# Optimization experiments

Measured on AMD Instinct MI355X. Metric: run time of the kernel, lower is better.

## Reference

```python
import jax, jax.numpy as jnp
import numpy as np

T, NP, NA, NV = 8, 16000, 16000, 200
DIN, H, KA, L = 256, 256, 4, 5
YEARS_TRAIN = (5, 6, 7)
BETA, EPS = 0.5, 1.0
SQRT2 = 1.4142135623730951


def setup_inputs() -> dict:
    key = jax.random.key(0)
    ks = jax.random.split(key, 24)
    s = 0.05
    return {
        'x_paper': jax.random.normal(ks[0], (T, NP, DIN), jnp.float32),
        'x_author': jax.random.normal(ks[1], (T, NA, DIN), jnp.float32),
        'x_venue': jax.random.normal(ks[2], (T, NV, DIN), jnp.float32),
        'neigh_author_idx': jax.random.randint(ks[3], (NP, KA), 0, NA),
        'neigh_venue_idx': jax.random.randint(ks[4], (NP,), 0, NV),
        'y_true': jax.random.uniform(ks[5], (len(YEARS_TRAIN), NP, L), jnp.float32, 0.0, 50.0),
        'W_paper': s * jax.random.normal(ks[6], (DIN, H), jnp.float32),
        'b_paper': jnp.zeros((H,), jnp.float32),
        'W_author': s * jax.random.normal(ks[7], (DIN, H), jnp.float32),
        'b_author': jnp.zeros((H,), jnp.float32),
        'W_venue': s * jax.random.normal(ks[8], (DIN, H), jnp.float32),
        'b_venue': jnp.zeros((H,), jnp.float32),
        'w_meta': jax.random.normal(ks[9], (3,), jnp.float32),
        'Wx': s * jax.random.normal(ks[10], (H, 3 * H), jnp.float32),
        'Wh': s * jax.random.normal(ks[11], (H, 3 * H), jnp.float32),
        'b_gru': jnp.zeros((3 * H,), jnp.float32),
        'W_eta': s * jax.random.normal(ks[12], (H, 1), jnp.float32),
        'b_eta': jnp.zeros((1,), jnp.float32),
        'W_mu': s * jax.random.normal(ks[13], (H, 1), jnp.float32),
        'b_mu': jnp.zeros((1,), jnp.float32),
        'W_sigma': s * jax.random.normal(ks[14], (H, 1), jnp.float32),
        'b_sigma': jnp.zeros((1,), jnp.float32),
    }


def reference(x_paper, x_author, x_venue, neigh_author_idx, neigh_venue_idx, y_true,
              W_paper, b_paper, W_author, b_author, W_venue, b_venue, w_meta,
              Wx, Wh, b_gru, W_eta, b_eta, W_mu, b_mu, W_sigma, b_sigma):
    # --- encoder: per-type linear + ReLU over all T snapshots ---
    emb_p = jax.nn.relu(jnp.einsum('tnd,dh->tnh', x_paper, W_paper) + b_paper)   # [T,NP,H]
    emb_a = jax.nn.relu(jnp.einsum('tnd,dh->tnh', x_author, W_author) + b_author)  # [T,NA,H]
    emb_v = jax.nn.relu(jnp.einsum('tnd,dh->tnh', x_venue, W_venue) + b_venue)   # [T,NV,H]

    # --- temporal smoothing regulariser L_time (all nodes common across years) ---
    l_time = jnp.mean(jnp.stack([
        jnp.mean(jnp.sum((e[1:] - e[:-1]) ** 2, axis=-1)) for e in (emb_p, emb_a, emb_v)
    ]))

    # --- weighted imputer, batched over all papers and all years ---
    w = jax.nn.softmax(w_meta)
    auth_mean = jnp.mean(emb_a[:, neigh_author_idx], axis=2)   # [T,NP,H]
    ven = emb_v[:, neigh_venue_idx]                            # [T,NP,H]
    v_all = w[0] * auth_mean + w[1] * ven + w[2] * emb_p       # [T,NP,H]

    # --- build lookback sequences V_p for all train years at once ---
    yrs = np.array([[t - k for k in range(1, L + 1)] for t in YEARS_TRAIN])  # [3,L]
    V = jnp.transpose(v_all[yrs], (0, 2, 1, 3)).reshape(-1, L, H)  # [B=3*NP, L, H]
    B = V.shape[0]

    # --- ImpactRNN: GRU over the lookback sequence ---
    def gru_step(h, x):
        gx = x @ Wx + b_gru
        gh = h @ Wh
        xr, xz, xn = jnp.split(gx, 3, axis=-1)
        hr, hz, hn = jnp.split(gh, 3, axis=-1)
        r = jax.nn.sigmoid(xr + hr)
        z = jax.nn.sigmoid(xz + hz)
        n = jnp.tanh(xn + r * hn)
        return (1.0 - z) * n + z * h, None

    h0 = jnp.zeros((B, H), V.dtype)
    h_last, _ = jax.lax.scan(gru_step, h0, jnp.swapaxes(V, 0, 1))

    eta = jax.nn.softplus(h_last @ W_eta + b_eta)              # [B,1]
    mu = h_last @ W_mu + b_mu                                  # [B,1]
    sigma = jax.nn.softplus(h_last @ W_sigma + b_sigma) + 1e-3  # [B,1]

    # --- cumulative log-normal citation curve, then per-horizon increments ---
    horizons = jnp.arange(1.0, L + 1.0, dtype=V.dtype)
    zscore = (jnp.log(horizons)[None, :] - mu) / (sigma * SQRT2)
    y_cum = eta * 0.5 * (1.0 + jax.lax.erf(zscore))            # [B,L]
    y_hat = jnp.concatenate([y_cum[:, :1], y_cum[:, 1:] - y_cum[:, :-1]], axis=1)

    l_pred = jnp.mean((jnp.log1p(y_true.reshape(-1, L) + EPS) - jnp.log1p(y_hat)) ** 2)
    return l_pred + BETA * l_time
```

## Files before the change

kernel.cpp:

```cpp
#include <hip/hip_runtime.h>
#include <cmath>

#define NP  16000
#define NV  200
#define HH  256

typedef short short8 __attribute__((ext_vector_type(8)));
typedef float f32x4  __attribute__((ext_vector_type(4)));

__device__ __forceinline__ unsigned short f2b(float f) {
  union { float f; unsigned u; } x; x.f = f;
  unsigned r = x.u + 0x7fffu + ((x.u >> 16) & 1u);
  return (unsigned short)(r >> 16);
}
__device__ __forceinline__ float b2f(unsigned short h) {
  union { unsigned u; float f; } x; x.u = ((unsigned)h) << 16;
  return x.f;
}
__device__ __forceinline__ float b2f_lo(unsigned u) {
  union { unsigned v; float f; } x; x.v = u << 16; return x.f;
}
__device__ __forceinline__ float b2f_hi(unsigned u) {
  union { unsigned v; float f; } x; x.v = u & 0xffff0000u; return x.f;
}
__device__ __forceinline__ unsigned cvt2(float a, float b) {
  unsigned r;
  asm("v_cvt_pk_bf16_f32 %0, %1, %2" : "=v"(r) : "v"(a), "v"(b));
  return r;
}
__device__ __forceinline__ void gld16(const void* g, void* l) {
  __builtin_amdgcn_global_load_lds((const __attribute__((address_space(1))) void*)g,
                                   (__attribute__((address_space(3))) void*)l, 16, 0, 0);
}
__device__ __forceinline__ float sigm(float x) { return 1.f / (1.f + __expf(-x)); }
__device__ __forceinline__ float tanhfast(float x) {
  const float e = __expf(-2.f * fabsf(x));
  const float t = (1.f - e) / (1.f + e);
  return x < 0.f ? -t : t;
}
__device__ __forceinline__ int xcd_swz(int orig, int q, int r) {
  const int xcd = orig & 7, loc = orig >> 3;
  return (xcd < r ? xcd * (q + 1) : r * (q + 1) + (xcd - r) * q) + loc;
}

__global__ __launch_bounds__(256) void packWt(const float* __restrict__ W,
                                              unsigned short* __restrict__ Wt) {
  const int n = blockIdx.x, k = threadIdx.x;
  Wt[n * 256 + k] = f2b(W[k * 256 + n]);
}
__global__ __launch_bounds__(256) void packW2t(const float* __restrict__ Wx,
                                               const float* __restrict__ Wh,
                                               unsigned short* __restrict__ W2t) {
  const int col = blockIdx.x;
  for (int k = threadIdx.x; k < 512; k += 256)
    W2t[(size_t)col * 512 + k] =
        f2b(k < 256 ? Wx[(size_t)k * 768 + col] : Wh[(size_t)(k - 256) * 768 + col]);
}

__global__ __launch_bounds__(512) void embed_all(
    const float* __restrict__ Xp, const float* __restrict__ Xa, const float* __restrict__ Xv,
    const unsigned short* __restrict__ Wtp, const unsigned short* __restrict__ Wta,
    const unsigned short* __restrict__ Wtv,
    const float* __restrict__ bp, const float* __restrict__ ba, const float* __restrict__ bvn,
    unsigned short* __restrict__ Ep, unsigned short* __restrict__ Ea,
    unsigned short* __restrict__ Ev) {
  __shared__ __align__(16) unsigned short lds[20480];
  unsigned short* As = lds;
  unsigned short* Bs = lds + 4096;
  const int t = threadIdx.x, w = t >> 6, l = t & 63;
  const int bid = blockIdx.x;
  const float* Xf; const unsigned short* Wt; const float* bias; unsigned short* E;
  int m0;
  if (bid < 2000)      { Xf = Xp; Wt = Wtp; bias = bp;  E = Ep; m0 = bid * 64; }
  else if (bid < 4000) { Xf = Xa; Wt = Wta; bias = ba;  E = Ea; m0 = (bid - 2000) * 64; }
  else                 { Xf = Xv; Wt = Wtv; bias = bvn; E = Ev; m0 = (bid - 4000) * 64; }
  const int srow = l >> 3, scol = ((l & 7) ^ srow) * 8;
  const int wrow = (w >> 2) * 32, wcol = (w & 3) * 64;
  const int arow = t >> 3, aseg = t & 7;
  const float* aptr = Xf + (size_t)(m0 + arow) * 256 + aseg * 8;

  f32x4 acc[2][4];
#pragma unroll
  for (int i = 0; i < 2; ++i)
#pragma unroll
    for (int j = 0; j < 4; ++j) acc[i][j] = {0.f, 0.f, 0.f, 0.f};

  float4 a0 = *reinterpret_cast<const float4*>(aptr);
  float4 a1 = *reinterpret_cast<const float4*>(aptr + 4);

#pragma unroll
  for (int c = 0; c < 4; ++c) {
#pragma unroll
    for (int i = 0; i < 4; ++i) {
      const int seg = 4 * w + i;
      gld16(Wt + (size_t)(8 * seg + srow) * 256 + c * 64 + scol, (void*)(Bs + seg * 512));
    }
    {
      uint4 u;
      u.x = cvt2(a0.x, a0.y); u.y = cvt2(a0.z, a0.w);
      u.z = cvt2(a1.x, a1.y); u.w = cvt2(a1.z, a1.w);
      const int slot = aseg ^ (arow & 7);
      *reinterpret_cast<uint4*>(As + arow * 64 + slot * 8) = u;
    }
    if (c < 3) {
      const float* np = aptr + (c + 1) * 64;
      a0 = *reinterpret_cast<const float4*>(np);
      a1 = *reinterpret_cast<const float4*>(np + 4);
    }
    __syncthreads();
#pragma unroll
    for (int ks = 0; ks < 2; ++ks) {
      short8 av[2], bv[4];
#pragma unroll
      for (int mi = 0; mi < 2; ++mi) {
        const int r = wrow + mi * 16 + (l & 15);
        const int slot = (ks * 4 + (l >> 4)) ^ (r & 7);
        av[mi] = *reinterpret_cast<const short8*>(As + r * 64 + slot * 8);
      }
#pragma unroll
      for (int nj = 0; nj < 4; ++nj) {
        const int r = wcol + nj * 16 + (l & 15);
        const int slot = (ks * 4 + (l >> 4)) ^ (r & 7);
        bv[nj] = *reinterpret_cast<const short8*>(Bs + r * 64 + slot * 8);
      }
#pragma unroll
      for (int mi = 0; mi < 2; ++mi)
#pragma unroll
        for (int nj = 0; nj < 4; ++nj)
          acc[mi][nj] = __builtin_amdgcn_mfma_f32_16x16x32_bf16(av[mi], bv[nj], acc[mi][nj], 0, 0, 0);
    }
    __syncthreads();
  }

#pragma unroll
  for (int nj = 0; nj < 4; ++nj) {
    const int col = wcol + nj * 16 + (l & 15);
    const float bvv = bias[col];
#pragma unroll
    for (int mi = 0; mi < 2; ++mi)
#pragma unroll
      for (int e = 0; e < 4; ++e) {
        const int row = wrow + mi * 16 + (l >> 4) * 4 + e;
        lds[row * 264 + col] = f2b(fmaxf(acc[mi][nj][e] + bvv, 0.f));
      }
  }
  __syncthreads();
  {
    const int r2 = t >> 3, s2 = t & 7;
    const unsigned short* src = lds + r2 * 264 + s2 * 32;
    const uint4 v0 = *reinterpret_cast<const uint4*>(src);
    const uint4 v1 = *reinterpret_cast<const uint4*>(src + 8);
    const uint4 v2 = *reinterpret_cast<const uint4*>(src + 16);
    const uint4 v3 = *reinterpret_cast<const uint4*>(src + 24);
    uint4* dst = reinterpret_cast<uint4*>(E + (size_t)(m0 + r2) * 256 + s2 * 32);
    dst[0] = v0; dst[1] = v1; dst[2] = v2; dst[3] = v3;
  }
}

__global__ __launch_bounds__(512) void gx_gemm(const unsigned short* __restrict__ Abf,
                                               const unsigned short* __restrict__ W2t,
                                               const float* __restrict__ bias,
                                               unsigned short* __restrict__ GX) {
  __shared__ __align__(16) unsigned short lds[20480];
  unsigned short* As = lds;
  unsigned short* Bs = lds + 4096;
  const int t = threadIdx.x, w = t >> 6, l = t & 63;
  const int work = xcd_swz(blockIdx.x, 656, 2);
  const int m0 = (work / 3) * 64, n0 = (work % 3) * 256;
  const int srow = l >> 3, scol = ((l & 7) ^ srow) * 8;
  const int wrow = (w >> 2) * 32, wcol = (w & 3) * 64;

  f32x4 acc[2][4];
#pragma unroll
  for (int i = 0; i < 2; ++i)
#pragma unroll
    for (int j = 0; j < 4; ++j) acc[i][j] = {0.f, 0.f, 0.f, 0.f};

#pragma unroll
  for (int c = 0; c < 4; ++c) {
    gld16(Abf + (size_t)(m0 + 8 * w + srow) * 256 + c * 64 + scol, (void*)(As + w * 512));
#pragma unroll
    for (int i = 0; i < 4; ++i) {
      const int seg = 4 * w + i;
      gld16(W2t + (size_t)(n0 + 8 * seg + srow) * 512 + c * 64 + scol, (void*)(Bs + seg * 512));
    }
    __syncthreads();
#pragma unroll
    for (int ks = 0; ks < 2; ++ks) {
      short8 av[2], bv[4];
#pragma unroll
      for (int mi = 0; mi < 2; ++mi) {
        const int r = wrow + mi * 16 + (l & 15);
        const int slot = (ks * 4 + (l >> 4)) ^ (r & 7);
        av[mi] = *reinterpret_cast<const short8*>(As + r * 64 + slot * 8);
      }
#pragma unroll
      for (int nj = 0; nj < 4; ++nj) {
        const int r = wcol + nj * 16 + (l & 15);
        const int slot = (ks * 4 + (l >> 4)) ^ (r & 7);
        bv[nj] = *reinterpret_cast<const short8*>(Bs + r * 64 + slot * 8);
      }
#pragma unroll
      for (int mi = 0; mi < 2; ++mi)
#pragma unroll
        for (int nj = 0; nj < 4; ++nj)
          acc[mi][nj] = __builtin_amdgcn_mfma_f32_16x16x32_bf16(av[mi], bv[nj], acc[mi][nj], 0, 0, 0);
    }
    __syncthreads();
  }

#pragma unroll
  for (int nj = 0; nj < 4; ++nj) {
    const int col = wcol + nj * 16 + (l & 15);
    const float bvv = bias[n0 + col];
#pragma unroll
    for (int mi = 0; mi < 2; ++mi)
#pragma unroll
      for (int e = 0; e < 4; ++e) {
        const int row = wrow + mi * 16 + (l >> 4) * 4 + e;
        lds[row * 264 + col] = f2b(acc[mi][nj][e] + bvv);
      }
  }
  __syncthreads();
  {
    const int r2 = t >> 3, s2 = t & 7;
    const unsigned short* src = lds + r2 * 264 + s2 * 32;
    const uint4 v0 = *reinterpret_cast<const uint4*>(src);
    const uint4 v1 = *reinterpret_cast<const uint4*>(src + 8);
    const uint4 v2 = *reinterpret_cast<const uint4*>(src + 16);
    const uint4 v3 = *reinterpret_cast<const uint4*>(src + 24);
    uint4* dst = reinterpret_cast<uint4*>(GX + (size_t)(m0 + r2) * 768 + n0 + s2 * 32);
    dst[0] = v0; dst[1] = v1; dst[2] = v2; dst[3] = v3;
  }
}

__global__ __launch_bounds__(256) void ltime_kernel(const unsigned short* __restrict__ ep,
                                                    const unsigned short* __restrict__ ea,
                                                    const unsigned short* __restrict__ ev,
                                                    float* __restrict__ partials) {
  const unsigned PO = 3584000u, VO = 44800u;
  const unsigned TOT = 2u * PO + VO;
  const unsigned SL = 512000u, SLV = 6400u;
  const float wbig = 1.f / (3.f * 7.f * 16000.f);
  const float wsmall = 1.f / (3.f * 7.f * 200.f);
  float local = 0.f;
  for (unsigned i = blockIdx.x * 256u + threadIdx.x; i < TOT; i += gridDim.x * 256u) {
    const unsigned short* base; unsigned off, sl; float wgt;
    if (i < 2u * PO) { base = (i < PO) ? ep : ea; off = (i < PO) ? i : i - PO; sl = SL; wgt = wbig; }
    else             { base = ev; off = i - 2u * PO; sl = SLV; wgt = wsmall; }
    const uint4 u0 = *reinterpret_cast<const uint4*>(base + (size_t)off * 8);
    const uint4 u1 = *reinterpret_cast<const uint4*>(base + (size_t)(off + sl) * 8);
    float s = 0.f, d;
    d = b2f_lo(u1.x) - b2f_lo(u0.x); s += d * d;
    d = b2f_hi(u1.x) - b2f_hi(u0.x); s += d * d;
    d = b2f_lo(u1.y) - b2f_lo(u0.y); s += d * d;
    d = b2f_hi(u1.y) - b2f_hi(u0.y); s += d * d;
    d = b2f_lo(u1.z) - b2f_lo(u0.z); s += d * d;
    d = b2f_hi(u1.z) - b2f_hi(u0.z); s += d * d;
    d = b2f_lo(u1.w) - b2f_lo(u0.w); s += d * d;
    d = b2f_hi(u1.w) - b2f_hi(u0.w); s += d * d;
    local += wgt * s;
  }
  __shared__ float red[256];
  red[threadIdx.x] = local;
  __syncthreads();
  for (int s = 128; s > 0; s >>= 1) {
    if (threadIdx.x < s) red[threadIdx.x] += red[threadIdx.x + s];
    __syncthreads();
  }
  if (threadIdx.x == 0) partials[blockIdx.x] = red[0];
}

__global__ __launch_bounds__(256) void vall_kernel(const unsigned short* __restrict__ ep,
                                                   const unsigned short* __restrict__ ea,
                                                   const unsigned short* __restrict__ ev,
                                                   const int* __restrict__ aidx,
                                                   const int* __restrict__ vidx,
                                                   const float* __restrict__ wm,
                                                   unsigned short* __restrict__ vall) {
  const int w = threadIdx.x >> 6, l = threadIdx.x & 63;
  const int n = blockIdx.x * 4 + w;
  float w0 = wm[0], w1 = wm[1], w2 = wm[2];
  const float mx = fmaxf(w0, fmaxf(w1, w2));
  const float e0 = expf(w0 - mx), e1 = expf(w1 - mx), e2 = expf(w2 - mx);
  const float inv = 1.f / (e0 + e1 + e2);
  w0 = e0 * inv; w1 = e1 * inv; w2 = e2 * inv;
  const int a0 = aidx[n * 4 + 0], a1 = aidx[n * 4 + 1];
  const int a2 = aidx[n * 4 + 2], a3 = aidx[n * 4 + 3];
  const int vn = vidx[n];
  const int cb = l * 4;
  for (int t = 0; t < 7; ++t) {
    const size_t tb = (size_t)t * NP * HH;
    const uint2 ua0 = *reinterpret_cast<const uint2*>(ea + tb + (size_t)a0 * HH + cb);
    const uint2 ua1 = *reinterpret_cast<const uint2*>(ea + tb + (size_t)a1 * HH + cb);
    const uint2 ua2 = *reinterpret_cast<const uint2*>(ea + tb + (size_t)a2 * HH + cb);
    const uint2 ua3 = *reinterpret_cast<const uint2*>(ea + tb + (size_t)a3 * HH + cb);
    const uint2 uv  = *reinterpret_cast<const uint2*>(ev + (size_t)t * NV * HH + (size_t)vn * HH + cb);
    const uint2 up  = *reinterpret_cast<const uint2*>(ep + tb + (size_t)n * HH + cb);
    float o[4];
    o[0] = w0 * 0.25f * (b2f_lo(ua0.x) + b2f_lo(ua1.x) + b2f_lo(ua2.x) + b2f_lo(ua3.x)) + w1 * b2f_lo(uv.x) + w2 * b2f_lo(up.x);
    o[1] = w0 * 0.25f * (b2f_hi(ua0.x) + b2f_hi(ua1.x) + b2f_hi(ua2.x) + b2f_hi(ua3.x)) + w1 * b2f_hi(uv.x) + w2 * b2f_hi(up.x);
    o[2] = w0 * 0.25f * (b2f_lo(ua0.y) + b2f_lo(ua1.y) + b2f_lo(ua2.y) + b2f_lo(ua3.y)) + w1 * b2f_lo(uv.y) + w2 * b2f_lo(up.y);
    o[3] = w0 * 0.25f * (b2f_hi(ua0.y) + b2f_hi(ua1.y) + b2f_hi(ua2.y) + b2f_hi(ua3.y)) + w1 * b2f_hi(uv.y) + w2 * b2f_hi(up.y);
    uint2 ov; ov.x = cvt2(o[0], o[1]); ov.y = cvt2(o[2], o[3]);
    *reinterpret_cast<uint2*>(vall + tb + (size_t)n * HH + cb) = ov;
  }
}

__global__ __launch_bounds__(256) void gru_h0(const unsigned short* __restrict__ GX,
                                              unsigned short* __restrict__ H0) {
  const int idx = blockIdx.x * 256 + threadIdx.x;
  const int hrow = idx >> 6, jq = idx & 63;
  const int g = (hrow >= 32000) ? 2 : (hrow >= 16000 ? 1 : 0);
  const int n = hrow - g * 16000;
  const size_t gxrow = (size_t)(4 + g) * 16000 + n;
  const unsigned short* gp = GX + gxrow * 768 + jq * 4;
  const uint2 uz = *reinterpret_cast<const uint2*>(gp + 256);
  const uint2 un = *reinterpret_cast<const uint2*>(gp + 512);
  float h[4];
  h[0] = (1.f - sigm(b2f_lo(uz.x))) * tanhfast(b2f_lo(un.x));
  h[1] = (1.f - sigm(b2f_hi(uz.x))) * tanhfast(b2f_hi(un.x));
  h[2] = (1.f - sigm(b2f_lo(uz.y))) * tanhfast(b2f_lo(un.y));
  h[3] = (1.f - sigm(b2f_hi(uz.y))) * tanhfast(b2f_hi(un.y));
  uint2 o; o.x = cvt2(h[0], h[1]); o.y = cvt2(h[2], h[3]);
  *reinterpret_cast<uint2*>(H0 + (size_t)hrow * 256 + jq * 4) = o;
}

__global__ __launch_bounds__(512, 2) void gru_hstep(const unsigned short* __restrict__ GX,
                                                    const unsigned short* __restrict__ W2t,
                                                    const unsigned short* __restrict__ Hsrc,
                                                    unsigned short* __restrict__ Hdst,
                                                    int lstep) {
  __shared__ __align__(16) unsigned short lds[32768];
  unsigned short* As = lds;
  unsigned short* Bs = lds + 8192;
  const int t = threadIdx.x, w = t >> 6, l = t & 63;
  const int work = xcd_swz(blockIdx.x, 93, 6);
  const int bx = work >> 1, jb = work & 1;
  const int m0 = bx * 128, j0 = jb * 128;
  const int g = bx / 125;
  const size_t gxRowBase = (size_t)(4 + g - lstep) * 16000 + (size_t)(m0 - g * 16000);
  const int srow = l >> 3;
  const int scol = ((l & 7) ^ srow) * 8;
  const int wr = w >> 2, wj = w & 3;
  f32x4 acc[3][4][2];
#pragma unroll
  for (int gate = 0; gate < 3; ++gate)
#pragma unroll
    for (int mi = 0; mi < 4; ++mi)
#pragma unroll
      for (int nj = 0; nj < 2; ++nj) acc[gate][mi][nj] = {0.f, 0.f, 0.f, 0.f};

#pragma unroll
  for (int c = 0; c < 4; ++c) {
#pragma unroll
    for (int i = 0; i < 2; ++i) {
      const int seg = w * 2 + i;
      gld16(Hsrc + (size_t)(m0 + 8 * seg + srow) * 256 + c * 64 + scol, (void*)(As + seg * 512));
    }
#pragma unroll
    for (int i = 0; i < 6; ++i) {
      const int seg = w * 6 + i;
      const int tilerow = 8 * seg + srow;
      const int gate = tilerow >> 7, jj = tilerow & 127;
      gld16(W2t + (size_t)(gate * 256 + j0 + jj) * 512 + 256 + c * 64 + scol,
            (void*)(Bs + seg * 512));
    }
    __syncthreads();
#pragma unroll
    for (int ks = 0; ks < 2; ++ks) {
      short8 av[4];
#pragma unroll
      for (int mi = 0; mi < 4; ++mi) {
        const int r = wr * 64 + mi * 16 + (l & 15);
        const int slot = (ks * 4 + (l >> 4)) ^ (r & 7);
        av[mi] = *reinterpret_cast<const short8*>(As + r * 64 + slot * 8);
      }
#pragma unroll
      for (int gate = 0; gate < 3; ++gate) {
        short8 bv0, bv1;
        {
          const int r0 = gate * 128 + wj * 32 + (l & 15);
          const int s0 = (ks * 4 + (l >> 4)) ^ (r0 & 7);
          bv0 = *reinterpret_cast<const short8*>(Bs + r0 * 64 + s0 * 8);
          const int r1 = r0 + 16;
          const int s1 = (ks * 4 + (l >> 4)) ^ (r1 & 7);
          bv1 = *reinterpret_cast<const short8*>(Bs + r1 * 64 + s1 * 8);
        }
#pragma unroll
        for (int mi = 0; mi < 4; ++mi) {
          acc[gate][mi][0] = __builtin_amdgcn_mfma_f32_16x16x32_bf16(av[mi], bv0, acc[gate][mi][0], 0, 0, 0);
          acc[gate][mi][1] = __builtin_amdgcn_mfma_f32_16x16x32_bf16(av[mi], bv1, acc[gate][mi][1], 0, 0, 0);
        }
      }
    }
    __syncthreads();
  }
  unsigned short* ep = lds + w * 2560;
#pragma unroll
  for (int nj = 0; nj < 2; ++nj) {
    const int jcol = j0 + wj * 32 + nj * 16 + (l & 15);
#pragma unroll
    for (int mi = 0; mi < 4; ++mi) {
#pragma unroll
      for (int e = 0; e < 4; ++e) {
        const int rib = wr * 64 + mi * 16 + (l >> 4) * 4 + e;
        const size_t hidx = (size_t)(m0 + rib) * 256 + jcol;
        const size_t gxoff = (gxRowBase + rib) * 768 + jcol;
        const float aR = acc[0][mi][nj][e] + b2f(GX[gxoff]);
        const float aZ = acc[1][mi][nj][e] + b2f(GX[gxoff + 256]);
        const float hn = acc[2][mi][nj][e];
        const float xn = b2f(GX[gxoff + 512]);
        const float rg = sigm(aR);
        const float zg = sigm(aZ);
        const float ng = tanhfast(xn + rg * hn);
        const float ho = b2f(Hsrc[hidx]);
        const int rl = mi * 16 + (l >> 4) * 4 + e;
        ep[rl * 40 + nj * 16 + (l & 15)] = f2b((1.f - zg) * ng + zg * ho);
      }
    }
  }
  __syncthreads();
  {
    const int grow = m0 + wr * 64 + l;
#pragma unroll
    for (int j = 0; j < 4; ++j) {
      const uint4 v = *reinterpret_cast<const uint4*>(ep + l * 40 + j * 8);
      *reinterpret_cast<uint4*>(Hdst + (size_t)grow * 256 + j0 + wj * 32 + j * 8) = v;
    }
  }
}

__device__ inline float softplusf(float x) { return x > 20.f ? x : log1pf(expf(x)); }

__global__ __launch_bounds__(256) void head_kernel(const unsigned short* __restrict__ Hbuf,
                                                   const float* __restrict__ We, const float* __restrict__ be,
                                                   const float* __restrict__ Wm, const float* __restrict__ bmu,
                                                   const float* __restrict__ Ws, const float* __restrict__ bsg,
                                                   const float* __restrict__ yt,
                                                   float* __restrict__ partials) {
  __shared__ float sWe[256], sWm[256], sWs[256];
  const int t = threadIdx.x;
  sWe[t] = We[t]; sWm[t] = Wm[t]; sWs[t] = Ws[t];
  __syncthreads();
  const int row = blockIdx.x * 256 + t;
  float loss = 0.f;
  if (row < 48000) {
    const unsigned short* h = Hbuf + (size_t)row * HH;
    float pe = 0.f, pm = 0.f, ps = 0.f;
#pragma unroll 4
    for (int k0 = 0; k0 < 256; k0 += 8) {
      const uint4 u = *reinterpret_cast<const uint4*>(h + k0);
      const float hv[8] = {b2f_lo(u.x), b2f_hi(u.x), b2f_lo(u.y), b2f_hi(u.y),
                           b2f_lo(u.z), b2f_hi(u.z), b2f_lo(u.w), b2f_hi(u.w)};
#pragma unroll
      for (int q = 0; q < 8; ++q) {
        const int k = k0 + q;
        pe += hv[q] * sWe[k]; pm += hv[q] * sWm[k]; ps += hv[q] * sWs[k];
      }
    }
    const float eta = softplusf(pe + be[0]);
    const float mu  = pm + bmu[0];
    const float sg  = softplusf(ps + bsg[0]) + 0.001f;
    const float inv = 1.f / (sg * 1.41421356237309515f);
    float prev = 0.f;
#pragma unroll
    for (int hz = 1; hz <= 5; ++hz) {
      const float z  = (logf((float)hz) - mu) * inv;
      const float yc = eta * 0.5f * (1.f + erff(z));
      const float yh = yc - prev; prev = yc;
      const float d  = log1pf(yt[(size_t)row * 5 + (hz - 1)] + 1.0f) - log1pf(yh);
      loss += d * d;
    }
  }
  __shared__ float red[256];
  red[t] = loss;
  __syncthreads();
  for (int s = 128; s > 0; s >>= 1) {
    if (t < s) red[t] += red[t + s];
    __syncthreads();
  }
  if (t == 0) partials[blockIdx.x] = red[0];
}

__global__ __launch_bounds__(256) void final_kernel(const float* __restrict__ lt,
                                                    const float* __restrict__ lp,
                                                    float* __restrict__ out) {
  __shared__ float r1[256], r2[256];
  float s1 = 0.f, s2 = 0.f;
  for (int i = threadIdx.x; i < 1024; i += 256) s1 += lt[i];
  for (int i = threadIdx.x; i < 188; i += 256) s2 += lp[i];
  r1[threadIdx.x] = s1; r2[threadIdx.x] = s2;
  __syncthreads();
  for (int s = 128; s > 0; s >>= 1) {
    if (threadIdx.x < s) { r1[threadIdx.x] += r1[threadIdx.x + s]; r2[threadIdx.x] += r2[threadIdx.x + s]; }
    __syncthreads();
  }
  if (threadIdx.x == 0) out[0] = r2[0] / 240000.f + 0.5f * r1[0];
}

extern "C" void kernel_launch(void* const* d_in, const int* in_sizes, int n_in,
                              void* d_out, int out_size, void* d_ws, size_t ws_size,
                              hipStream_t stream) {
  (void)in_sizes; (void)n_in; (void)out_size; (void)ws_size;
  const float* x_paper  = (const float*)d_in[0];
  const float* x_author = (const float*)d_in[1];
  const float* x_venue  = (const float*)d_in[2];
  const int*   aidx     = (const int*)d_in[3];
  const int*   vidx     = (const int*)d_in[4];
  const float* y_true   = (const float*)d_in[5];
  const float* W_paper  = (const float*)d_in[6];
  const float* b_paper  = (const float*)d_in[7];
  const float* W_author = (const float*)d_in[8];
  const float* b_author = (const float*)d_in[9];
  const float* W_venue  = (const float*)d_in[10];
  const float* b_venue  = (const float*)d_in[11];
  const float* w_meta   = (const float*)d_in[12];
  const float* Wx       = (const float*)d_in[13];
  const float* Wh       = (const float*)d_in[14];
  const float* b_gru    = (const float*)d_in[15];
  const float* W_eta    = (const float*)d_in[16];
  const float* b_eta    = (const float*)d_in[17];
  const float* W_mu     = (const float*)d_in[18];
  const float* b_mu     = (const float*)d_in[19];
  const float* W_sigma  = (const float*)d_in[20];
  const float* b_sigma  = (const float*)d_in[21];

  unsigned short* p = (unsigned short*)d_ws;
  unsigned short* va16 = p;  p += (size_t)7 * NP * 256;
  unsigned short* Hb0  = p;  p += (size_t)48000 * 256;
  unsigned short* Hb1  = p;  p += (size_t)48000 * 256;
  unsigned short* W2t  = p;  p += (size_t)768 * 512;
  unsigned short* GX   = p;  p += (size_t)112000 * 768;
  float* ltp = (float*)p;
  float* lpp = ltp + 1024;
  unsigned short* ep16 = GX;
  unsigned short* ea16 = ep16 + (size_t)8 * NP * 256;
  unsigned short* ev16 = ea16 + (size_t)8 * NP * 256;
  unsigned short* Wtp  = ev16 + (size_t)8 * NV * 256;
  unsigned short* Wta  = Wtp + 65536;
  unsigned short* Wtv  = Wta + 65536;

  packWt<<<256, 256, 0, stream>>>(W_paper,  Wtp);
  packWt<<<256, 256, 0, stream>>>(W_author, Wta);
  packWt<<<256, 256, 0, stream>>>(W_venue,  Wtv);
  packW2t<<<768, 256, 0, stream>>>(Wx, Wh, W2t);

  embed_all<<<4025, 512, 0, stream>>>(x_paper, x_author, x_venue, Wtp, Wta, Wtv,
                                      b_paper, b_author, b_venue, ep16, ea16, ev16);

  ltime_kernel<<<1024, 256, 0, stream>>>(ep16, ea16, ev16, ltp);
  vall_kernel<<<NP / 4, 256, 0, stream>>>(ep16, ea16, ev16, aidx, vidx, w_meta, va16);

  gx_gemm<<<5250, 512, 0, stream>>>(va16, W2t, b_gru, GX);

  gru_h0<<<12000, 256, 0, stream>>>(GX, Hb0);
  gru_hstep<<<750, 512, 0, stream>>>(GX, W2t, Hb0, Hb1, 1);
  gru_hstep<<<750, 512, 0, stream>>>(GX, W2t, Hb1, Hb0, 2);
  gru_hstep<<<750, 512, 0, stream>>>(GX, W2t, Hb0, Hb1, 3);
  gru_hstep<<<750, 512, 0, stream>>>(GX, W2t, Hb1, Hb0, 4);

  head_kernel<<<188, 256, 0, stream>>>(Hb0, W_eta, b_eta, W_mu, b_mu, W_sigma, b_sigma,
                                       y_true, lpp);
  final_kernel<<<1, 256, 0, stream>>>(ltp, lpp, (float*)d_out);
}
```

Baseline: 558.7 us.

## Double-buffer LDS in embed and gx GEMMs; merge weight pack kernels

The embed_all and gx_gemm kernels now double-buffer their LDS tiles. The next K-chunk's global loads are issued before the MFMA work on the current chunk, so each iteration needs one barrier instead of a wait-then-compute pattern. The four weight-packing launches are merged into a single pack_all kernel to cut launch overhead. In exchange, LDS per block doubles to 80 KB, which may reduce how many blocks fit on each CU.

```diff
diff --git a/kernel.cpp b/kernel.cpp
--- a/kernel.cpp
+++ b/kernel.cpp
@@ -43,18 +43,27 @@
   return (xcd < r ? xcd * (q + 1) : r * (q + 1) + (xcd - r) * q) + loc;
 }
 
-__global__ __launch_bounds__(256) void packWt(const float* __restrict__ W,
-                                              unsigned short* __restrict__ Wt) {
-  const int n = blockIdx.x, k = threadIdx.x;
-  Wt[n * 256 + k] = f2b(W[k * 256 + n]);
-}
-__global__ __launch_bounds__(256) void packW2t(const float* __restrict__ Wx,
-                                               const float* __restrict__ Wh,
-                                               unsigned short* __restrict__ W2t) {
-  const int col = blockIdx.x;
-  for (int k = threadIdx.x; k < 512; k += 256)
-    W2t[(size_t)col * 512 + k] =
-        f2b(k < 256 ? Wx[(size_t)k * 768 + col] : Wh[(size_t)(k - 256) * 768 + col]);
+__global__ __launch_bounds__(256) void pack_all(const float* __restrict__ Wp,
+                                                const float* __restrict__ Wa,
+                                                const float* __restrict__ Wv,
+                                                const float* __restrict__ Wx,
+                                                const float* __restrict__ Wh,
+                                                unsigned short* __restrict__ Wtp,
+                                                unsigned short* __restrict__ Wta,
+                                                unsigned short* __restrict__ Wtv,
+                                                unsigned short* __restrict__ W2t) {
+  const int b = blockIdx.x, k = threadIdx.x;
+  if (b < 768) {
+    const float* W = b < 256 ? Wp : (b < 512 ? Wa : Wv);
+    unsigned short* Wt = b < 256 ? Wtp : (b < 512 ? Wta : Wtv);
+    const int n = b & 255;
+    Wt[n * 256 + k] = f2b(W[k * 256 + n]);
+  } else {
+    const int col = b - 768;
+    for (int kk = k; kk < 512; kk += 256)
+      W2t[(size_t)col * 512 + kk] =
+          f2b(kk < 256 ? Wx[(size_t)kk * 768 + col] : Wh[(size_t)(kk - 256) * 768 + col]);
+  }
 }
 
 __global__ __launch_bounds__(512) void embed_all(
@@ -64,9 +73,7 @@
     const float* __restrict__ bp, const float* __restrict__ ba, const float* __restrict__ bvn,
     unsigned short* __restrict__ Ep, unsigned short* __restrict__ Ea,
     unsigned short* __restrict__ Ev) {
-  __shared__ __align__(16) unsigned short lds[20480];
-  unsigned short* As = lds;
-  unsigned short* Bs = lds + 4096;
+  __shared__ __align__(16) unsigned short lds[40960];
   const int t = threadIdx.x, w = t >> 6, l = t & 63;
   const int bid = blockIdx.x;
   const float* Xf; const unsigned short* Wt; const float* bias; unsigned short* E;
@@ -78,6 +85,7 @@
   const int wrow = (w >> 2) * 32, wcol = (w & 3) * 64;
   const int arow = t >> 3, aseg = t & 7;
   const float* aptr = Xf + (size_t)(m0 + arow) * 256 + aseg * 8;
+  const int aslot = aseg ^ (arow & 7);
 
   f32x4 acc[2][4];
 #pragma unroll
@@ -85,29 +93,38 @@
 #pragma unroll
     for (int j = 0; j < 4; ++j) acc[i][j] = {0.f, 0.f, 0.f, 0.f};
 
-  float4 a0 = *reinterpret_cast<const float4*>(aptr);
-  float4 a1 = *reinterpret_cast<const float4*>(aptr + 4);
-
-#pragma unroll
-  for (int c = 0; c < 4; ++c) {
+  {
+    const float4 a0 = *reinterpret_cast<const float4*>(aptr);
+    const float4 a1 = *reinterpret_cast<const float4*>(aptr + 4);
 #pragma unroll
     for (int i = 0; i < 4; ++i) {
       const int seg = 4 * w + i;
-      gld16(Wt + (size_t)(8 * seg + srow) * 256 + c * 64 + scol, (void*)(Bs + seg * 512));
-    }
-    {
-      uint4 u;
-      u.x = cvt2(a0.x, a0.y); u.y = cvt2(a0.z, a0.w);
-      u.z = cvt2(a1.x, a1.y); u.w = cvt2(a1.z, a1.w);
-      const int slot = aseg ^ (arow & 7);
-      *reinterpret_cast<uint4*>(As + arow * 64 + slot * 8) = u;
-    }
+      gld16(Wt + (size_t)(8 * seg + srow) * 256 + scol, (void*)(lds + 4096 + seg * 512));
+    }
+    uint4 u;
+    u.x = cvt2(a0.x, a0.y); u.y = cvt2(a0.z, a0.w);
+    u.z = cvt2(a1.x, a1.y); u.w = cvt2(a1.z, a1.w);
+    *reinterpret_cast<uint4*>(lds + arow * 64 + aslot * 8) = u;
+  }
+  __syncthreads();
+
+#pragma unroll
+  for (int c = 0; c < 4; ++c) {
+    unsigned short* As = lds + (c & 1) * 20480;
+    unsigned short* Bs = As + 4096;
+    unsigned short* Asn = lds + ((c + 1) & 1) * 20480;
+    unsigned short* Bsn = Asn + 4096;
+    float4 a0, a1;
     if (c < 3) {
       const float* np = aptr + (c + 1) * 64;
       a0 = *reinterpret_cast<const float4*>(np);
       a1 = *reinterpret_cast<const float4*>(np + 4);
-    }
-    __syncthreads();
+#pragma unroll
+      for (int i = 0; i < 4; ++i) {
+        const int seg = 4 * w + i;
+        gld16(Wt + (size_t)(8 * seg + srow) * 256 + (c + 1) * 64 + scol, (void*)(Bsn + seg * 512));
+      }
+    }
 #pragma unroll
     for (int ks = 0; ks < 2; ++ks) {
       short8 av[2], bv[4];
@@ -127,7 +144,14 @@
       for (int mi = 0; mi < 2; ++mi)
 #pragma unroll
         for (int nj = 0; nj < 4; ++nj)
-          acc[mi][nj] = __builtin_amdgcn_mfma_f32_16x16x32_bf16(av[mi], bv[nj], acc[mi][nj], 0, 0, 0);
+          acc[mi][nj] = __builtin_amdgcn_mfma_f32_16x16x32_bf16(av[ks == 0 ? mi : mi], bv[nj], acc[mi][nj], 0, 0, 0),
+          (void)0;
+    }
+    if (c < 3) {
+      uint4 u;
+      u.x = cvt2(a0.x, a0.y); u.y = cvt2(a0.z, a0.w);
+      u.z = cvt2(a1.x, a1.y); u.w = cvt2(a1.z, a1.w);
+      *reinterpret_cast<uint4*>(Asn + arow * 64 + aslot * 8) = u;
     }
     __syncthreads();
   }
@@ -161,9 +185,7 @@
                                                const unsigned short* __restrict__ W2t,
                                                const float* __restrict__ bias,
                                                unsigned short* __restrict__ GX) {
-  __shared__ __align__(16) unsigned short lds[20480];
-  unsigned short* As = lds;
-  unsigned short* Bs = lds + 4096;
+  __shared__ __align__(16) unsigned short lds[40960];
   const int t = threadIdx.x, w = t >> 6, l = t & 63;
   const int work = xcd_swz(blockIdx.x, 656, 2);
   const int m0 = (work / 3) * 64, n0 = (work % 3) * 256;
@@ -176,15 +198,29 @@
 #pragma unroll
     for (int j = 0; j < 4; ++j) acc[i][j] = {0.f, 0.f, 0.f, 0.f};
 
+  gld16(Abf + (size_t)(m0 + 8 * w + srow) * 256 + scol, (void*)(lds + w * 512));
+#pragma unroll
+  for (int i = 0; i < 4; ++i) {
+    const int seg = 4 * w + i;
+    gld16(W2t + (size_t)(n0 + 8 * seg + srow) * 512 + scol, (void*)(lds + 4096 + seg * 512));
+  }
+  __syncthreads();
+
 #pragma unroll
   for (int c = 0; c < 4; ++c) {
-    gld16(Abf + (size_t)(m0 + 8 * w + srow) * 256 + c * 64 + scol, (void*)(As + w * 512));
-#pragma unroll
-    for (int i = 0; i < 4; ++i) {
-      const int seg = 4 * w + i;
-      gld16(W2t + (size_t)(n0 + 8 * seg + srow) * 512 + c * 64 + scol, (void*)(Bs + seg * 512));
-    }
-    __syncthreads();
+    unsigned short* As = lds + (c & 1) * 20480;
+    unsigned short* Bs = As + 4096;
+    unsigned short* Asn = lds + ((c + 1) & 1) * 20480;
+    unsigned short* Bsn = Asn + 4096;
+    if (c < 3) {
+      gld16(Abf + (size_t)(m0 + 8 * w + srow) * 256 + (c + 1) * 64 + scol, (void*)(Asn + w * 512));
+#pragma unroll
+      for (int i = 0; i < 4; ++i) {
+        const int seg = 4 * w + i;
+        gld16(W2t + (size_t)(n0 + 8 * seg + srow) * 512 + (c + 1) * 64 + scol,
+              (void*)(Bsn + seg * 512));
+      }
+    }
 #pragma unroll
     for (int ks = 0; ks < 2; ++ks) {
       short8 av[2], bv[4];
@@ -541,10 +577,8 @@
   unsigned short* Wta  = Wtp + 65536;
   unsigned short* Wtv  = Wta + 65536;
 
-  packWt<<<256, 256, 0, stream>>>(W_paper,  Wtp);
-  packWt<<<256, 256, 0, stream>>>(W_author, Wta);
-  packWt<<<256, 256, 0, stream>>>(W_venue,  Wtv);
-  packW2t<<<768, 256, 0, stream>>>(Wx, Wh, W2t);
+  pack_all<<<1536, 256, 0, stream>>>(W_paper, W_author, W_venue, Wx, Wh,
+                                     Wtp, Wta, Wtv, W2t);
 
   embed_all<<<4025, 512, 0, stream>>>(x_paper, x_author, x_venue, Wtp, Wta, Wtv,
                                       b_paper, b_author, b_venue, ep16, ea16, ev16);
```

New measurement: 573.8 us. 1.03x slower.

## Fuse temporal-smoothness loss into venue/author aggregation kernel and merge pack kernels

Applied to the files above, without the earlier changes.

Merges the separate l_time reduction kernel into the meta-path aggregation kernel so each paper row's embedding is read once for both the smoothness term and the weighted sum. Author and venue temporal diffs are computed in the same blocks, and the partial count grows to 4000. The four weight-packing launches are also merged into one. This removes a full extra pass over the paper embeddings and some launch overhead, at the cost of a larger final reduction and extra per-block author-row reads.

```diff
diff --git a/kernel.cpp b/kernel.cpp
--- a/kernel.cpp
+++ b/kernel.cpp
@@ -43,18 +43,27 @@
   return (xcd < r ? xcd * (q + 1) : r * (q + 1) + (xcd - r) * q) + loc;
 }
 
-__global__ __launch_bounds__(256) void packWt(const float* __restrict__ W,
-                                              unsigned short* __restrict__ Wt) {
-  const int n = blockIdx.x, k = threadIdx.x;
-  Wt[n * 256 + k] = f2b(W[k * 256 + n]);
-}
-__global__ __launch_bounds__(256) void packW2t(const float* __restrict__ Wx,
-                                               const float* __restrict__ Wh,
-                                               unsigned short* __restrict__ W2t) {
-  const int col = blockIdx.x;
-  for (int k = threadIdx.x; k < 512; k += 256)
-    W2t[(size_t)col * 512 + k] =
-        f2b(k < 256 ? Wx[(size_t)k * 768 + col] : Wh[(size_t)(k - 256) * 768 + col]);
+__global__ __launch_bounds__(256) void pack_all(const float* __restrict__ Wp,
+                                                const float* __restrict__ Wa,
+                                                const float* __restrict__ Wv,
+                                                const float* __restrict__ Wx,
+                                                const float* __restrict__ Wh,
+                                                unsigned short* __restrict__ Wtp,
+                                                unsigned short* __restrict__ Wta,
+                                                unsigned short* __restrict__ Wtv,
+                                                unsigned short* __restrict__ W2t) {
+  const int b = blockIdx.x, k = threadIdx.x;
+  if (b < 768) {
+    const float* W = b < 256 ? Wp : (b < 512 ? Wa : Wv);
+    unsigned short* Wt = b < 256 ? Wtp : (b < 512 ? Wta : Wtv);
+    const int n = b & 255;
+    Wt[n * 256 + k] = f2b(W[k * 256 + n]);
+  } else {
+    const int col = b - 768;
+    for (int kk = k; kk < 512; kk += 256)
+      W2t[(size_t)col * 512 + kk] =
+          f2b(kk < 256 ? Wx[(size_t)kk * 768 + col] : Wh[(size_t)(kk - 256) * 768 + col]);
+  }
 }
 
 __global__ __launch_bounds__(512) void embed_all(
@@ -157,6 +166,93 @@
   }
 }
 
+__global__ __launch_bounds__(256) void ltvall_kernel(
+    const unsigned short* __restrict__ ep, const unsigned short* __restrict__ ea,
+    const unsigned short* __restrict__ ev,
+    const int* __restrict__ aidx, const int* __restrict__ vidx,
+    const float* __restrict__ wm,
+    unsigned short* __restrict__ vall, float* __restrict__ partials) {
+  const int w = threadIdx.x >> 6, l = threadIdx.x & 63;
+  const int n = blockIdx.x * 4 + w;
+  const int cb = l * 4;
+  float w0 = wm[0], w1 = wm[1], w2 = wm[2];
+  const float mx = fmaxf(w0, fmaxf(w1, w2));
+  const float e0 = expf(w0 - mx), e1 = expf(w1 - mx), e2 = expf(w2 - mx);
+  const float inv = 1.f / (e0 + e1 + e2);
+  w0 = e0 * inv; w1 = e1 * inv; w2 = e2 * inv;
+  const int a0 = aidx[n * 4 + 0], a1 = aidx[n * 4 + 1];
+  const int a2 = aidx[n * 4 + 2], a3 = aidx[n * 4 + 3];
+  const int vn = vidx[n];
+  const float wbig = 1.f / (3.f * 7.f * 16000.f);
+  const float wsmall = 1.f / (3.f * 7.f * 200.f);
+  float lt = 0.f;
+
+  uint2 prevp;
+  for (int t = 0; t < 8; ++t) {
+    const size_t tb = (size_t)t * NP * HH;
+    const uint2 up = *reinterpret_cast<const uint2*>(ep + tb + (size_t)n * HH + cb);
+    if (t >= 1) {
+      float d;
+      d = b2f_lo(up.x) - b2f_lo(prevp.x); lt += wbig * d * d;
+      d = b2f_hi(up.x) - b2f_hi(prevp.x); lt += wbig * d * d;
+      d = b2f_lo(up.y) - b2f_lo(prevp.y); lt += wbig * d * d;
+      d = b2f_hi(up.y) - b2f_hi(prevp.y); lt += wbig * d * d;
+    }
+    if (t < 7) {
+      const uint2 ua0 = *reinterpret_cast<const uint2*>(ea + tb + (size_t)a0 * HH + cb);
+      const uint2 ua1 = *reinterpret_cast<const uint2*>(ea + tb + (size_t)a1 * HH + cb);
+      const uint2 ua2 = *reinterpret_cast<const uint2*>(ea + tb + (size_t)a2 * HH + cb);
+      const uint2 ua3 = *reinterpret_cast<const uint2*>(ea + tb + (size_t)a3 * HH + cb);
+      const uint2 uv  = *reinterpret_cast<const uint2*>(ev + ((size_t)t * NV + vn) * HH + cb);
+      float o[4];
+      o[0] = w0 * 0.25f * (b2f_lo(ua0.x) + b2f_lo(ua1.x) + b2f_lo(ua2.x) + b2f_lo(ua3.x)) + w1 * b2f_lo(uv.x) + w2 * b2f_lo(up.x);
+      o[1] = w0 * 0.25f * (b2f_hi(ua0.x) + b2f_hi(ua1.x) + b2f_hi(ua2.x) + b2f_hi(ua3.x)) + w1 * b2f_hi(uv.x) + w2 * b2f_hi(up.x);
+      o[2] = w0 * 0.25f * (b2f_lo(ua0.y) + b2f_lo(ua1.y) + b2f_lo(ua2.y) + b2f_lo(ua3.y)) + w1 * b2f_lo(uv.y) + w2 * b2f_lo(up.y);
+      o[3] = w0 * 0.25f * (b2f_hi(ua0.y) + b2f_hi(ua1.y) + b2f_hi(ua2.y) + b2f_hi(ua3.y)) + w1 * b2f_hi(uv.y) + w2 * b2f_hi(up.y);
+      uint2 ov; ov.x = cvt2(o[0], o[1]); ov.y = cvt2(o[2], o[3]);
+      *reinterpret_cast<uint2*>(vall + tb + (size_t)n * HH + cb) = ov;
+    }
+    prevp = up;
+  }
+  {
+    uint2 prva;
+    for (int t = 0; t < 8; ++t) {
+      const uint2 ua = *reinterpret_cast<const uint2*>(ea + ((size_t)t * NP + n) * HH + cb);
+      if (t >= 1) {
+        float d;
+        d = b2f_lo(ua.x) - b2f_lo(prva.x); lt += wbig * d * d;
+        d = b2f_hi(ua.x) - b2f_hi(prva.x); lt += wbig * d * d;
+        d = b2f_lo(ua.y) - b2f_lo(prva.y); lt += wbig * d * d;
+        d = b2f_hi(ua.y) - b2f_hi(prva.y); lt += wbig * d * d;
+      }
+      prva = ua;
+    }
+  }
+  if (blockIdx.x < 50) {
+    const int nv2 = blockIdx.x * 4 + w;
+    uint2 prvv;
+    for (int t = 0; t < 8; ++t) {
+      const uint2 uvv = *reinterpret_cast<const uint2*>(ev + ((size_t)t * NV + nv2) * HH + cb);
+      if (t >= 1) {
+        float d;
+        d = b2f_lo(uvv.x) - b2f_lo(prvv.x); lt += wsmall * d * d;
+        d = b2f_hi(uvv.x) - b2f_hi(prvv.x); lt += wsmall * d * d;
+        d = b2f_lo(uvv.y) - b2f_lo(prvv.y); lt += wsmall * d * d;
+        d = b2f_hi(uvv.y) - b2f_hi(prvv.y); lt += wsmall * d * d;
+      }
+      prvv = uvv;
+    }
+  }
+  __shared__ float red[256];
+  red[threadIdx.x] = lt;
+  __syncthreads();
+  for (int s = 128; s > 0; s >>= 1) {
+    if (threadIdx.x < s) red[threadIdx.x] += red[threadIdx.x + s];
+    __syncthreads();
+  }
+  if (threadIdx.x == 0) partials[blockIdx.x] = red[0];
+}
+
 __global__ __launch_bounds__(512) void gx_gemm(const unsigned short* __restrict__ Abf,
                                                const unsigned short* __restrict__ W2t,
                                                const float* __restrict__ bias,
@@ -231,79 +327,6 @@
     const uint4 v3 = *reinterpret_cast<const uint4*>(src + 24);
     uint4* dst = reinterpret_cast<uint4*>(GX + (size_t)(m0 + r2) * 768 + n0 + s2 * 32);
     dst[0] = v0; dst[1] = v1; dst[2] = v2; dst[3] = v3;
-  }
-}
-
-__global__ __launch_bounds__(256) void ltime_kernel(const unsigned short* __restrict__ ep,
-                                                    const unsigned short* __restrict__ ea,
-                                                    const unsigned short* __restrict__ ev,
-                                                    float* __restrict__ partials) {
-  const unsigned PO = 3584000u, VO = 44800u;
-  const unsigned TOT = 2u * PO + VO;
-  const unsigned SL = 512000u, SLV = 6400u;
-  const float wbig = 1.f / (3.f * 7.f * 16000.f);
-  const float wsmall = 1.f / (3.f * 7.f * 200.f);
-  float local = 0.f;
-  for (unsigned i = blockIdx.x * 256u + threadIdx.x; i < TOT; i += gridDim.x * 256u) {
-    const unsigned short* base; unsigned off, sl; float wgt;
-    if (i < 2u * PO) { base = (i < PO) ? ep : ea; off = (i < PO) ? i : i - PO; sl = SL; wgt = wbig; }
-    else             { base = ev; off = i - 2u * PO; sl = SLV; wgt = wsmall; }
-    const uint4 u0 = *reinterpret_cast<const uint4*>(base + (size_t)off * 8);
-    const uint4 u1 = *reinterpret_cast<const uint4*>(base + (size_t)(off + sl) * 8);
-    float s = 0.f, d;
-    d = b2f_lo(u1.x) - b2f_lo(u0.x); s += d * d;
-    d = b2f_hi(u1.x) - b2f_hi(u0.x); s += d * d;
-    d = b2f_lo(u1.y) - b2f_lo(u0.y); s += d * d;
-    d = b2f_hi(u1.y) - b2f_hi(u0.y); s += d * d;
-    d = b2f_lo(u1.z) - b2f_lo(u0.z); s += d * d;
-    d = b2f_hi(u1.z) - b2f_hi(u0.z); s += d * d;
-    d = b2f_lo(u1.w) - b2f_lo(u0.w); s += d * d;
-    d = b2f_hi(u1.w) - b2f_hi(u0.w); s += d * d;
-    local += wgt * s;
-  }
-  __shared__ float red[256];
-  red[threadIdx.x] = local;
-  __syncthreads();
-  for (int s = 128; s > 0; s >>= 1) {
-    if (threadIdx.x < s) red[threadIdx.x] += red[threadIdx.x + s];
-    __syncthreads();
-  }
-  if (threadIdx.x == 0) partials[blockIdx.x] = red[0];
-}
-
-__global__ __launch_bounds__(256) void vall_kernel(const unsigned short* __restrict__ ep,
-                                                   const unsigned short* __restrict__ ea,
-                                                   const unsigned short* __restrict__ ev,
-                                                   const int* __restrict__ aidx,
-                                                   const int* __restrict__ vidx,
-                                                   const float* __restrict__ wm,
-                                                   unsigned short* __restrict__ vall) {
-  const int w = threadIdx.x >> 6, l = threadIdx.x & 63;
-  const int n = blockIdx.x * 4 + w;
-  float w0 = wm[0], w1 = wm[1], w2 = wm[2];
-  const float mx = fmaxf(w0, fmaxf(w1, w2));
-  const float e0 = expf(w0 - mx), e1 = expf(w1 - mx), e2 = expf(w2 - mx);
-  const float inv = 1.f / (e0 + e1 + e2);
-  w0 = e0 * inv; w1 = e1 * inv; w2 = e2 * inv;
-  const int a0 = aidx[n * 4 + 0], a1 = aidx[n * 4 + 1];
-  const int a2 = aidx[n * 4 + 2], a3 = aidx[n * 4 + 3];
-  const int vn = vidx[n];
-  const int cb = l * 4;
-  for (int t = 0; t < 7; ++t) {
-    const size_t tb = (size_t)t * NP * HH;
-    const uint2 ua0 = *reinterpret_cast<const uint2*>(ea + tb + (size_t)a0 * HH + cb);
-    const uint2 ua1 = *reinterpret_cast<const uint2*>(ea + tb + (size_t)a1 * HH + cb);
-    const uint2 ua2 = *reinterpret_cast<const uint2*>(ea + tb + (size_t)a2 * HH + cb);
-    const uint2 ua3 = *reinterpret_cast<const uint2*>(ea + tb + (size_t)a3 * HH + cb);
-    const uint2 uv  = *reinterpret_cast<const uint2*>(ev + (size_t)t * NV * HH + (size_t)vn * HH + cb);
-    const uint2 up  = *reinterpret_cast<const uint2*>(ep + tb + (size_t)n * HH + cb);
-    float o[4];
-    o[0] = w0 * 0.25f * (b2f_lo(ua0.x) + b2f_lo(ua1.x) + b2f_lo(ua2.x) + b2f_lo(ua3.x)) + w1 * b2f_lo(uv.x) + w2 * b2f_lo(up.x);
-    o[1] = w0 * 0.25f * (b2f_hi(ua0.x) + b2f_hi(ua1.x) + b2f_hi(ua2.x) + b2f_hi(ua3.x)) + w1 * b2f_hi(uv.x) + w2 * b2f_hi(up.x);
-    o[2] = w0 * 0.25f * (b2f_lo(ua0.y) + b2f_lo(ua1.y) + b2f_lo(ua2.y) + b2f_lo(ua3.y)) + w1 * b2f_lo(uv.y) + w2 * b2f_lo(up.y);
-    o[3] = w0 * 0.25f * (b2f_hi(ua0.y) + b2f_hi(ua1.y) + b2f_hi(ua2.y) + b2f_hi(ua3.y)) + w1 * b2f_hi(uv.y) + w2 * b2f_hi(up.y);
-    uint2 ov; ov.x = cvt2(o[0], o[1]); ov.y = cvt2(o[2], o[3]);
-    *reinterpret_cast<uint2*>(vall + tb + (size_t)n * HH + cb) = ov;
   }
 }
 
@@ -488,7 +511,7 @@
                                                     float* __restrict__ out) {
   __shared__ float r1[256], r2[256];
   float s1 = 0.f, s2 = 0.f;
-  for (int i = threadIdx.x; i < 1024; i += 256) s1 += lt[i];
+  for (int i = threadIdx.x; i < 4000; i += 256) s1 += lt[i];
   for (int i = threadIdx.x; i < 188; i += 256) s2 += lp[i];
   r1[threadIdx.x] = s1; r2[threadIdx.x] = s2;
   __syncthreads();
@@ -533,7 +556,7 @@
   unsigned short* W2t  = p;  p += (size_t)768 * 512;
   unsigned short* GX   = p;  p += (size_t)112000 * 768;
   float* ltp = (float*)p;
-  float* lpp = ltp + 1024;
+  float* lpp = ltp + 4096;
   unsigned short* ep16 = GX;
   unsigned short* ea16 = ep16 + (size_t)8 * NP * 256;
   unsigned short* ev16 = ea16 + (size_t)8 * NP * 256;
@@ -541,16 +564,14 @@
   unsigned short* Wta  = Wtp + 65536;
   unsigned short* Wtv  = Wta + 65536;
 
-  packWt<<<256, 256, 0, stream>>>(W_paper,  Wtp);
-  packWt<<<256, 256, 0, stream>>>(W_author, Wta);
-  packWt<<<256, 256, 0, stream>>>(W_venue,  Wtv);
-  packW2t<<<768, 256, 0, stream>>>(Wx, Wh, W2t);
+  pack_all<<<1536, 256, 0, stream>>>(W_paper, W_author, W_venue, Wx, Wh,
+                                     Wtp, Wta, Wtv, W2t);
 
   embed_all<<<4025, 512, 0, stream>>>(x_paper, x_author, x_venue, Wtp, Wta, Wtv,
                                       b_paper, b_author, b_venue, ep16, ea16, ev16);
 
-  ltime_kernel<<<1024, 256, 0, stream>>>(ep16, ea16, ev16, ltp);
-  vall_kernel<<<NP / 4, 256, 0, stream>>>(ep16, ea16, ev16, aidx, vidx, w_meta, va16);
+  ltvall_kernel<<<4000, 256, 0, stream>>>(ep16, ea16, ev16, aidx, vidx, w_meta,
+                                          va16, ltp);
 
   gx_gemm<<<5250, 512, 0, stream>>>(va16, W2t, b_gru, GX);
 
```

Result: faster. 542.3 us (-2.9%).
